# Kernel optimization log

Hardware: AMD Instinct MI355X
Metric: run time of the kernel (lower is better)

## Reference

```python
import jax, jax.numpy as jnp
import numpy as np
import math

SEQ_LEN = 2048
D_MODEL = 512
HEADS = 8
HEAD_DIM = D_MODEL // HEADS
BATCH = 4


def setup_inputs() -> dict:
    key = jax.random.key(0)
    ks = jax.random.split(key, 12)
    s = 0.02
    return {
        "query": jax.random.normal(ks[0], (BATCH, SEQ_LEN, D_MODEL), dtype=jnp.float32),
        "Wq": jax.random.normal(ks[1], (D_MODEL, D_MODEL), dtype=jnp.float32) * s,
        "bq": jnp.zeros((D_MODEL,), dtype=jnp.float32),
        "Wk": jax.random.normal(ks[2], (D_MODEL, D_MODEL), dtype=jnp.float32) * s,
        "bk": jnp.zeros((D_MODEL,), dtype=jnp.float32),
        "Wv": jax.random.normal(ks[3], (D_MODEL, D_MODEL), dtype=jnp.float32) * s,
        "bv": jnp.zeros((D_MODEL,), dtype=jnp.float32),
        "Wp": jax.random.normal(ks[4], (D_MODEL, D_MODEL), dtype=jnp.float32) * s,
        "bp": jnp.zeros((D_MODEL,), dtype=jnp.float32),
        "logit_scale": jnp.full((HEADS, 1, 1), math.log(10.0), dtype=jnp.float32),
        "rpe": jax.random.normal(ks[5], (2 * SEQ_LEN - 1, HEADS), dtype=jnp.float32) * s,
    }


def reference(query, Wq, bq, Wk, bk, Wv, bv, Wp, bp, logit_scale, rpe):
    N, S, D = query.shape
    H = HEADS

    def split_heads(x):
        # reshape(N, S, head_dim, H) then permute(0, 3, 1, 2) -> (N, H, S, head_dim)
        return x.reshape(N, S, D // H, H).transpose(0, 3, 1, 2)

    q = split_heads(query @ Wq.T + bq)
    k = split_heads(query @ Wk.T + bk)  # key defaults to query
    v = split_heads(query @ Wv.T + bv)  # value defaults to key

    attn = jnp.einsum("bhqd,bhkd->bhqk", q, k) / math.sqrt(D)
    scale = jnp.exp(jnp.minimum(logit_scale, math.log(1.0 / 0.01)))  # (H,1,1)
    attn = attn * scale[None]

    # relative position bias: idx[i,j] = i - j + S - 1
    idx = jnp.arange(S)[:, None] - jnp.arange(S)[None, :] + (S - 1)  # (S,S)
    bias = jax.nn.sigmoid(rpe[idx].transpose(2, 0, 1))  # (H,S,S)
    attn = attn + bias[None]

    attn = jax.nn.softmax(attn, axis=-1)
    out = jnp.einsum("bhqk,bhkd->bhqd", attn, v)
    out = out.transpose(0, 2, 1, 3).reshape(N, S, D)
    return out @ Wp.T + bp
```

## Files before the change

kernel.cpp:

```cpp
#include <hip/hip_runtime.h>
#include <math.h>

#define N_B 4
#define SEQ 2048
#define DM  512
#define H_N 8
#define DH  64

typedef unsigned short ushort_t;
typedef __attribute__((ext_vector_type(8))) short short8_t;
typedef __attribute__((ext_vector_type(4))) float float4_t;

#define LOG2E 1.4426950408889634074f

__device__ __forceinline__ ushort_t f2bf(float f) {
    unsigned int x = __float_as_uint(f);
    unsigned int lsb = (x >> 16) & 1u;
    x += 0x7fffu + lsb;
    return (ushort_t)(x >> 16);
}
__device__ __forceinline__ unsigned int cvtpk_bf16(float a, float b) {
    unsigned int r;
    asm("v_cvt_pk_bf16_f32 %0, %1, %2" : "=v"(r) : "v"(a), "v"(b));
    return r;
}
__device__ __forceinline__ float fexp2(float x) {
#if __has_builtin(__builtin_amdgcn_exp2f)
    return __builtin_amdgcn_exp2f(x);
#else
    return exp2f(x);
#endif
}
__device__ __forceinline__ void gload_lds16(const ushort_t* g, ushort_t* l) {
    __builtin_amdgcn_global_load_lds((const __attribute__((address_space(1))) void*)g,
                                     (__attribute__((address_space(3))) void*)l,
                                     16, 0, 0);
}

#define Q4 1048576
#define W4 65536
#define RELN 4095
#define GTABN (H_N * RELN)
__global__ __launch_bounds__(256)
void prep(const float* __restrict__ query,
          const float* __restrict__ Wq, const float* __restrict__ Wk,
          const float* __restrict__ Wv, const float* __restrict__ Wp,
          const float* __restrict__ bq, const float* __restrict__ bk,
          const float* __restrict__ bv, const float* __restrict__ bp,
          const float* __restrict__ rpe,
          ushort_t* __restrict__ q16, ushort_t* __restrict__ w16,
          float* __restrict__ bcat, float* __restrict__ gtab)
{
    int i = blockIdx.x * 256 + threadIdx.x;
    if (i < Q4) {
        float4 x = ((const float4*)query)[i];
        uint2 p;
        p.x = cvtpk_bf16(x.x, x.y);
        p.y = cvtpk_bf16(x.z, x.w);
        ((uint2*)q16)[i] = p;
    } else if (i < Q4 + 4 * W4) {
        int wi = i - Q4;
        int w = wi >> 16;
        const float* W = (w == 0) ? Wq : (w == 1) ? Wk : (w == 2) ? Wv : Wp;
        float4 x = ((const float4*)W)[wi & (W4 - 1)];
        uint2 p;
        p.x = cvtpk_bf16(x.x, x.y);
        p.y = cvtpk_bf16(x.z, x.w);
        ((uint2*)w16)[wi] = p;
    } else if (i < Q4 + 4 * W4 + 512) {
        int bi = i - (Q4 + 4 * W4);
        int seg = bi >> 7;
        int off = bi & 127;
        const float* B = (seg == 0) ? bq : (seg == 1) ? bk : (seg == 2) ? bv : bp;
        ((float4*)bcat)[bi] = ((const float4*)B)[off];
    } else {
        int gi = i - (Q4 + 4 * W4 + 512);
        if (gi < GTABN) {
            int h = gi / RELN;
            int rel = gi - h * RELN;
            float4 v;
            #pragma unroll
            for (int c = 0; c < 4; c++) {
                int rr = rel - c;
                if (rr < 0) rr = 0;
                float x = rpe[rr * H_N + h];
                ((float*)&v)[c] = LOG2E / (1.0f + __expf(-x));
            }
            ((float4*)gtab)[gi] = v;
        }
    }
}

template<int MODE>
__global__ __launch_bounds__(256)
void mgemm(const ushort_t* __restrict__ A, const ushort_t* __restrict__ B,
           const float* __restrict__ bias,
           ushort_t* __restrict__ q_o, ushort_t* __restrict__ k_o,
           ushort_t* __restrict__ vt_o, float* __restrict__ p_o)
{
    __shared__ __align__(16) ushort_t As[128][64];
    __shared__ __align__(16) ushort_t Bs[128][64];

    const int t     = threadIdx.x;
    const int wid   = t >> 6;
    const int lane  = t & 63;
    const int lan16 = lane & 15;
    const int quad  = lane >> 4;
    const int wm    = (wid & 1) * 64;
    const int wn    = (wid >> 1) * 64;

    const int col0 = blockIdx.x * 128;
    const int row0 = blockIdx.y * 128;

    const int srow = lane >> 3;
    const int gchk = (lane & 7) ^ ((lane >> 3) & 7);
    const ushort_t* gA = A + (size_t)(row0 + wid * 8 + srow) * DM + gchk * 8;
    const ushort_t* gB = B + (size_t)(col0 + wid * 8 + srow) * DM + gchk * 8;

    float4_t acc[4][4];
    #pragma unroll
    for (int i = 0; i < 4; i++)
        #pragma unroll
        for (int j = 0; j < 4; j++) acc[i][j] = (float4_t){0.f, 0.f, 0.f, 0.f};

    const int sw = lan16 & 7;

    for (int k0 = 0; k0 < DM; k0 += 64) {
        __syncthreads();
        #pragma unroll
        for (int j = 0; j < 4; j++) {
            gload_lds16(gA + k0 + (size_t)j * 32 * DM, &As[j * 32 + wid * 8][0]);
            gload_lds16(gB + k0 + (size_t)j * 32 * DM, &Bs[j * 32 + wid * 8][0]);
        }
        asm volatile("s_waitcnt vmcnt(0)" ::: "memory");
        __syncthreads();

        #pragma unroll
        for (int kk = 0; kk < 2; kk++) {
            short8_t af[4], bf[4];
            #pragma unroll
            for (int i = 0; i < 4; i++) {
                af[i] = *(const short8_t*)&As[wm + i * 16 + lan16][((kk * 4 + quad) ^ sw) * 8];
                bf[i] = *(const short8_t*)&Bs[wn + i * 16 + lan16][((kk * 4 + quad) ^ sw) * 8];
            }
            #pragma unroll
            for (int i = 0; i < 4; i++)
                #pragma unroll
                for (int j = 0; j < 4; j++)
                    acc[i][j] = __builtin_amdgcn_mfma_f32_16x16x32_bf16(af[i], bf[j], acc[i][j], 0, 0, 0);
        }
    }

    #pragma unroll
    for (int j = 0; j < 4; j++) {
        int col = col0 + wn + j * 16 + lan16;
        float bv = bias[col];
        #pragma unroll
        for (int i = 0; i < 4; i++) {
            #pragma unroll
            for (int reg = 0; reg < 4; reg++) {
                int row = row0 + wm + i * 16 + quad * 4 + reg;
                float v = acc[i][j][reg] + bv;
                if (MODE == 0) {
                    int w = col >> 9;
                    int c = col & 511;
                    int hh = c & 7, dh = c >> 3;
                    int n = row >> 11, s = row & 2047;
                    if (w == 0)
                        q_o[(((size_t)(n * H_N + hh)) * SEQ + s) * DH + dh] = f2bf(v);
                    else if (w == 1)
                        k_o[(((size_t)(n * H_N + hh)) * SEQ + s) * DH + dh] = f2bf(v);
                    else
                        vt_o[(((size_t)(n * H_N + hh)) * DH + dh) * SEQ + s] = f2bf(v);
                } else {
                    p_o[(size_t)row * DM + col] = v;
                }
            }
        }
    }
}

__global__ __launch_bounds__(512)
void attn_k(const ushort_t* __restrict__ qw, const ushort_t* __restrict__ kw,
            const ushort_t* __restrict__ vt, const float* __restrict__ lsc,
            const float* __restrict__ gtab, ushort_t* __restrict__ ctx)
{
    __shared__ __align__(16) ushort_t K_s[64][72];
    __shared__ __align__(16) ushort_t VT_s[64][72];
    __shared__ __align__(16) unsigned int Pp[8][16][36];

    const int t     = threadIdx.x;
    const int wid   = t >> 6;
    const int lane  = t & 63;
    const int lan16 = lane & 15;
    const int quad  = lane >> 4;

    const int h  = blockIdx.x;
    const int qt = blockIdx.y;
    const int n  = blockIdx.z;
    const int q0 = qt * 128;

    const size_t headoff = ((size_t)(n * H_N + h)) * SEQ * DH;
    const ushort_t* qh  = qw + headoff;
    const ushort_t* kh  = kw + headoff;
    const ushort_t* vth = vt + headoff;

    float ls = lsc[h];
    const float lm = 4.60517018598809136804f;
    if (ls > lm) ls = lm;
    const float scale2 = __expf(ls) * 0.04419417382415921757f * LOG2E;

    const int qrow = q0 + wid * 16 + lan16;
    const float4* gt = (const float4*)gtab + (size_t)h * RELN + (qrow + 2047 - quad * 4);

    short8_t qb[2];
    {
        const ushort_t* src = qh + (size_t)qrow * DH + quad * 8;
        qb[0] = *(const short8_t*)(src);
        qb[1] = *(const short8_t*)(src + 32);
    }

    float l_run = 0.f;
    float4_t o[4];
    #pragma unroll
    for (int ds = 0; ds < 4; ds++) o[ds] = (float4_t){0.f, 0.f, 0.f, 0.f};

    const int srow = t >> 3;
    const int sc16 = (t & 7) * 8;

    for (int j0 = 0; j0 < SEQ; j0 += 64) {
        float4 b4[4];
        {
            const float4* gtp = gt - j0;
            #pragma unroll
            for (int sub = 0; sub < 4; sub++) b4[sub] = gtp[-(sub * 16)];
        }

        __syncthreads();
        {
            const ushort_t* ksrc = kh + (size_t)(j0 + srow) * DH + sc16;
            *(uint4*)&K_s[srow][sc16] = *(const uint4*)(ksrc);
            const ushort_t* vsrc = vth + (size_t)srow * SEQ + j0 + sc16;
            *(uint4*)&VT_s[srow][sc16] = *(const uint4*)(vsrc);
        }
        __syncthreads();

        float4_t st[4];
        #pragma unroll
        for (int sub = 0; sub < 4; sub++) {
            const ushort_t* kp = &K_s[sub * 16 + lan16][quad * 8];
            short8_t ka0 = *(const short8_t*)(kp);
            short8_t ka1 = *(const short8_t*)(kp + 32);
            float4_t a = (float4_t){0.f, 0.f, 0.f, 0.f};
            a = __builtin_amdgcn_mfma_f32_16x16x32_bf16(ka0, qb[0], a, 0, 0, 0);
            a = __builtin_amdgcn_mfma_f32_16x16x32_bf16(ka1, qb[1], a, 0, 0, 0);
            st[sub] = a;
        }

        {
            float ps = 0.f;
            #pragma unroll
            for (int sub = 0; sub < 4; sub++) {
                float e0 = fexp2(st[sub][0] * scale2 + b4[sub].x);
                float e1 = fexp2(st[sub][1] * scale2 + b4[sub].y);
                float e2 = fexp2(st[sub][2] * scale2 + b4[sub].z);
                float e3 = fexp2(st[sub][3] * scale2 + b4[sub].w);
                ps += (e0 + e1) + (e2 + e3);
                uint2 pw;
                pw.x = cvtpk_bf16(e0, e1);
                pw.y = cvtpk_bf16(e2, e3);
                *(uint2*)&Pp[wid][lan16][sub * 8 + quad * 2] = pw;
            }
            l_run += ps;
        }
        asm volatile("s_waitcnt lgkmcnt(0)" ::: "memory");

        #pragma unroll
        for (int ks = 0; ks < 2; ks++) {
            short8_t pb = *(const short8_t*)&Pp[wid][lan16][ks * 16 + quad * 4];
            #pragma unroll
            for (int ds = 0; ds < 4; ds++) {
                short8_t va = *(const short8_t*)&VT_s[ds * 16 + lan16][ks * 32 + quad * 8];
                o[ds] = __builtin_amdgcn_mfma_f32_16x16x32_bf16(va, pb, o[ds], 0, 0, 0);
            }
        }
    }

    {
        float l = l_run;
        l += __shfl_xor(l, 16);
        l += __shfl_xor(l, 32);
        float inv = 1.0f / l;
        size_t base = ((size_t)n * SEQ + qrow) * DM + h * DH;
        #pragma unroll
        for (int ds = 0; ds < 4; ds++) {
            uint2 p;
            p.x = cvtpk_bf16(o[ds][0] * inv, o[ds][1] * inv);
            p.y = cvtpk_bf16(o[ds][2] * inv, o[ds][3] * inv);
            *(uint2*)(ctx + base + ds * 16 + quad * 4) = p;
        }
    }
}

extern "C" void kernel_launch(void* const* d_in, const int* in_sizes, int n_in,
                              void* d_out, int out_size, void* d_ws, size_t ws_size,
                              hipStream_t stream) {
    const float* query = (const float*)d_in[0];
    const float* Wq  = (const float*)d_in[1];
    const float* bq  = (const float*)d_in[2];
    const float* Wk  = (const float*)d_in[3];
    const float* bk  = (const float*)d_in[4];
    const float* Wv  = (const float*)d_in[5];
    const float* bv  = (const float*)d_in[6];
    const float* Wp  = (const float*)d_in[7];
    const float* bp  = (const float*)d_in[8];
    const float* lsc = (const float*)d_in[9];
    const float* rpe = (const float*)d_in[10];

    const size_t QEL = (size_t)N_B * SEQ * DM;
    const size_t WEL = (size_t)DM * DM;
    char* ws = (char*)d_ws;
    ushort_t* q16  = (ushort_t*)(ws);
    ushort_t* w16  = q16 + QEL;
    float*    bcat = (float*)(w16 + 4 * WEL);
    float*    gtab = bcat + 2048;
    ushort_t* qb   = (ushort_t*)(gtab + 4 * GTABN);
    ushort_t* kb   = qb + QEL;
    ushort_t* vtb  = kb + QEL;
    ushort_t* ctx  = vtb + QEL;

    const int PREPN = Q4 + 4 * W4 + 512 + GTABN;
    prep<<<(PREPN + 255) / 256, 256, 0, stream>>>(
        query, Wq, Wk, Wv, Wp, bq, bk, bv, bp, rpe, q16, w16, bcat, gtab);

    dim3 g1(1536 / 128, (N_B * SEQ) / 128);
    mgemm<0><<<g1, 256, 0, stream>>>(q16, w16, bcat, qb, kb, vtb, nullptr);

    dim3 ga(H_N, SEQ / 128, N_B);
    attn_k<<<ga, 512, 0, stream>>>(qb, kb, vtb, lsc, gtab, ctx);

    dim3 g2(DM / 128, (N_B * SEQ) / 128);
    mgemm<1><<<g2, 256, 0, stream>>>(ctx, w16 + 3 * WEL, bcat + 1536,
                                     nullptr, nullptr, nullptr, (float*)d_out);
}
```

Baseline: 212.1 us.

## Double-buffer K/V tiles in LDS with register prefetch of next tile

The attention kernel now loads the next K and V^T tiles and the bias-table values into registers at the start of each iteration. These are written into an alternate shared-memory buffer after the compute, which leaves one barrier per iteration instead of two. This is meant to hide global-load latency behind the MFMA and exp work. The cost is doubled LDS for the K/V tiles and extra registers, which could reduce occupancy.

```diff
diff --git a/kernel.cpp b/kernel.cpp
--- a/kernel.cpp
+++ b/kernel.cpp
@@ -185,8 +185,8 @@
             const ushort_t* __restrict__ vt, const float* __restrict__ lsc,
             const float* __restrict__ gtab, ushort_t* __restrict__ ctx)
 {
-    __shared__ __align__(16) ushort_t K_s[64][72];
-    __shared__ __align__(16) ushort_t VT_s[64][72];
+    __shared__ __align__(16) ushort_t K_s[2][64][72];
+    __shared__ __align__(16) ushort_t VT_s[2][64][72];
     __shared__ __align__(16) unsigned int Pp[8][16][36];
 
     const int t     = threadIdx.x;
@@ -227,28 +227,34 @@
 
     const int srow = t >> 3;
     const int sc16 = (t & 7) * 8;
+    const ushort_t* kbase = kh + (size_t)srow * DH + sc16;
+    const ushort_t* vbase = vth + (size_t)srow * SEQ + sc16;
+
+    uint4 kreg = *(const uint4*)(kbase);
+    uint4 vreg = *(const uint4*)(vbase);
+    float4 b4c[4];
+    #pragma unroll
+    for (int sub = 0; sub < 4; sub++) b4c[sub] = gt[-(sub * 16)];
+    *(uint4*)&K_s[0][srow][sc16]  = kreg;
+    *(uint4*)&VT_s[0][srow][sc16] = vreg;
+    __syncthreads();
+    int cur = 0;
 
     for (int j0 = 0; j0 < SEQ; j0 += 64) {
-        float4 b4[4];
-        {
-            const float4* gtp = gt - j0;
-            #pragma unroll
-            for (int sub = 0; sub < 4; sub++) b4[sub] = gtp[-(sub * 16)];
-        }
-
-        __syncthreads();
-        {
-            const ushort_t* ksrc = kh + (size_t)(j0 + srow) * DH + sc16;
-            *(uint4*)&K_s[srow][sc16] = *(const uint4*)(ksrc);
-            const ushort_t* vsrc = vth + (size_t)srow * SEQ + j0 + sc16;
-            *(uint4*)&VT_s[srow][sc16] = *(const uint4*)(vsrc);
-        }
-        __syncthreads();
+        const bool more = (j0 + 64 < SEQ);
+        float4 b4n[4];
+        if (more) {
+            kreg = *(const uint4*)(kbase + (size_t)(j0 + 64) * DH);
+            vreg = *(const uint4*)(vbase + (j0 + 64));
+            const float4* gtp = gt - (j0 + 64);
+            #pragma unroll
+            for (int sub = 0; sub < 4; sub++) b4n[sub] = gtp[-(sub * 16)];
+        }
 
         float4_t st[4];
         #pragma unroll
         for (int sub = 0; sub < 4; sub++) {
-            const ushort_t* kp = &K_s[sub * 16 + lan16][quad * 8];
+            const ushort_t* kp = &K_s[cur][sub * 16 + lan16][quad * 8];
             short8_t ka0 = *(const short8_t*)(kp);
             short8_t ka1 = *(const short8_t*)(kp + 32);
             float4_t a = (float4_t){0.f, 0.f, 0.f, 0.f};
@@ -261,10 +267,10 @@
             float ps = 0.f;
             #pragma unroll
             for (int sub = 0; sub < 4; sub++) {
-                float e0 = fexp2(st[sub][0] * scale2 + b4[sub].x);
-                float e1 = fexp2(st[sub][1] * scale2 + b4[sub].y);
-                float e2 = fexp2(st[sub][2] * scale2 + b4[sub].z);
-                float e3 = fexp2(st[sub][3] * scale2 + b4[sub].w);
+                float e0 = fexp2(st[sub][0] * scale2 + b4c[sub].x);
+                float e1 = fexp2(st[sub][1] * scale2 + b4c[sub].y);
+                float e2 = fexp2(st[sub][2] * scale2 + b4c[sub].z);
+                float e3 = fexp2(st[sub][3] * scale2 + b4c[sub].w);
                 ps += (e0 + e1) + (e2 + e3);
                 uint2 pw;
                 pw.x = cvtpk_bf16(e0, e1);
@@ -280,9 +286,18 @@
             short8_t pb = *(const short8_t*)&Pp[wid][lan16][ks * 16 + quad * 4];
             #pragma unroll
             for (int ds = 0; ds < 4; ds++) {
-                short8_t va = *(const short8_t*)&VT_s[ds * 16 + lan16][ks * 32 + quad * 8];
+                short8_t va = *(const short8_t*)&VT_s[cur][ds * 16 + lan16][ks * 32 + quad * 8];
                 o[ds] = __builtin_amdgcn_mfma_f32_16x16x32_bf16(va, pb, o[ds], 0, 0, 0);
             }
+        }
+
+        if (more) {
+            *(uint4*)&K_s[cur ^ 1][srow][sc16]  = kreg;
+            *(uint4*)&VT_s[cur ^ 1][srow][sc16] = vreg;
+            __syncthreads();
+            cur ^= 1;
+            #pragma unroll
+            for (int sub = 0; sub < 4; sub++) b4c[sub] = b4n[sub];
         }
     }
 
```

Measured after the change: 206.1 us. 1.03x faster.
